# Kernel optimization log

Measured on AMD Instinct MI355X. Metric: run time of the kernel, lower is better.

Reference implementation:

```python
import jax, jax.numpy as jnp
import numpy as np

B_, L, DM = 2, 2048, 1024
DI, N, K, R = 2048, 16, 4, 64  # d_inner, d_state, d_conv, dt_rank


def setup_inputs() -> dict:
    key = jax.random.key(0)
    ks = jax.random.split(key, 8)
    return {
        "x": jax.random.normal(ks[0], (B_, L, DM), jnp.float32),
        "W_in": jax.random.normal(ks[1], (DM, 2 * DI), jnp.float32) * 0.02,
        "w_conv": jax.random.normal(ks[2], (DI, K), jnp.float32) * 0.1,
        "b_conv": jnp.zeros((DI,), jnp.float32),
        "W_x": jax.random.normal(ks[3], (DI, R + 2 * N), jnp.float32) * 0.02,
        "W_dt": jax.random.normal(ks[4], (R, DI), jnp.float32) * 0.02,
        "b_dt": jnp.full((DI,), -4.6, jnp.float32),  # softplus(b_dt) ~ 0.01 dt init
        "A_log": jnp.log(jnp.broadcast_to(jnp.arange(1, N + 1, dtype=jnp.float32), (DI, N))),
        "D": jnp.ones((DI,), jnp.float32),
        "W_out": jax.random.normal(ks[5], (DI, DM), jnp.float32) * 0.02,
        "gamma": jnp.ones((DM,), jnp.float32),
        "beta": jnp.zeros((DM,), jnp.float32),
    }


def reference(x, W_in, w_conv, b_conv, W_x, W_dt, b_dt, A_log, D, W_out, gamma, beta):
    Bb, Ll, Dm = x.shape
    Di, Kk = w_conv.shape
    Nn = A_log.shape[1]
    Rr = W_dt.shape[0]
    # in_proj -> (u, z)
    xz = x @ W_in  # [B,L,2*Di]
    u, z = jnp.split(xz, 2, axis=-1)
    # depthwise causal conv1d (kernel K, left pad K-1) + SiLU
    up = jnp.pad(u, ((0, 0), (Kk - 1, 0), (0, 0)))
    conv = b_conv + sum(up[:, k:k + Ll, :] * w_conv[:, k] for k in range(Kk))
    u = jax.nn.silu(conv)  # [B,L,Di]
    # x_proj -> dt, B, C
    dbc = u @ W_x
    dt, Bm, Cm = dbc[..., :Rr], dbc[..., Rr:Rr + Nn], dbc[..., Rr + Nn:]
    delta = jax.nn.softplus(dt @ W_dt + b_dt)  # [B,L,Di]
    A = -jnp.exp(A_log)  # [Di,N]

    def step(h, inputs):
        d_t, B_t, C_t, u_t = inputs  # [B,Di],[B,N],[B,N],[B,Di]
        dA = jnp.exp(d_t[..., None] * A)            # [B,Di,N]
        h = h * dA + (d_t * u_t)[..., None] * B_t[:, None, :]
        y = jnp.einsum('bdn,bn->bd', h, C_t)
        return h, y

    h0 = jnp.zeros((Bb, Di, Nn), x.dtype)
    _, ys = jax.lax.scan(step, h0, (delta.transpose(1, 0, 2), Bm.transpose(1, 0, 2),
                                    Cm.transpose(1, 0, 2), u.transpose(1, 0, 2)))
    y = ys.transpose(1, 0, 2)        # [B,L,Di]
    y = y + u * D                    # skip term
    y = y * jax.nn.silu(z)           # gate
    out = y @ W_out                  # [B,L,Dm]
    # LayerNorm
    mu = out.mean(-1, keepdims=True)
    var = ((out - mu) ** 2).mean(-1, keepdims=True)
    out = (out - mu) * jax.lax.rsqrt(var + 1e-5) * gamma + beta
    # dropout p=0 -> identity; residual
    return out + x
```

## Files before the change

kernel.cpp:

```cpp
#include <hip/hip_runtime.h>
#include <math.h>

#define L_SEQ 2048
#define DMOD  1024
#define DIN   2048
#define NBATCH 2
#define NTOK  (NBATCH * L_SEQ)
#define NST   16
#define RRANK 64
#define LOG2E 1.44269504088896f

#define GCHUNK 128
#define CLEN   (L_SEQ / GCHUNK)
#define SCHUNK 8
#define NSTAGE (CLEN / SCHUNK)

#define G4_KS   4
#define G4_KC   (2048 / G4_KS)
#define G2_KS   16
#define G2_KC   (2048 / G2_KS)

typedef __attribute__((ext_vector_type(8))) short  short8;
typedef __attribute__((ext_vector_type(4))) float  f32x4;

__device__ __forceinline__ ushort f2bf(float f) {
    unsigned u = __float_as_uint(f);
    u += 0x7fffu + ((u >> 16) & 1u);
    return (ushort)(u >> 16);
}
__device__ __forceinline__ float bf2f(ushort u) {
    return __uint_as_float(((unsigned)u) << 16);
}
__device__ __forceinline__ float fexp2(float x) {
    return __builtin_amdgcn_exp2f(x);
}

__device__ __forceinline__ void gload16(const ushort* g, ushort* l) {
    __builtin_amdgcn_global_load_lds(
        (const __attribute__((address_space(1))) unsigned int*)g,
        (__attribute__((address_space(3))) unsigned int*)l,
        16, 0, 0);
}

__device__ __forceinline__ void cast_body(
    const float* __restrict__ src, ushort* __restrict__ dst, int bid, int tid)
{
    int i = (bid * 256 + tid) * 8;
    float4 a = *(const float4*)(src + i);
    float4 b = *(const float4*)(src + i + 4);
    ushort4 o0 = make_ushort4(f2bf(a.x), f2bf(a.y), f2bf(a.z), f2bf(a.w));
    ushort4 o1 = make_ushort4(f2bf(b.x), f2bf(b.y), f2bf(b.z), f2bf(b.w));
    *(ushort4*)(dst + i)     = o0;
    *(ushort4*)(dst + i + 4) = o1;
}

__device__ __forceinline__ void tcast_body(
    const float* __restrict__ src, ushort* __restrict__ dst,
    int R, int C, int bx, int by, int tid)
{
    __shared__ float t[32][33];
    int tx = tid & 31;
    int ty = tid >> 5;
    int c0 = bx * 32;
    int r0 = by * 32;
    #pragma unroll
    for (int i = 0; i < 4; ++i)
        t[ty + i * 8][tx] = src[(size_t)(r0 + ty + i * 8) * C + c0 + tx];
    __syncthreads();
    #pragma unroll
    for (int i = 0; i < 4; ++i)
        dst[(size_t)(c0 + ty + i * 8) * R + r0 + tx] = f2bf(t[tx][ty + i * 8]);
}

__global__ __launch_bounds__(256) void prep_k(
    const float* __restrict__ x, const float* __restrict__ W_in,
    const float* __restrict__ W_dt, const float* __restrict__ W_x,
    const float* __restrict__ W_out,
    ushort* __restrict__ xb, ushort* __restrict__ Wib,
    ushort* __restrict__ Wdtb, ushort* __restrict__ Wxb,
    ushort* __restrict__ Wob)
{
    int bid = blockIdx.x, tid = threadIdx.x;
    if (bid < 2048) {
        cast_body(x, xb, bid, tid);
    } else if (bid < 6144) {
        int t = bid - 2048;
        tcast_body(W_in, Wib, 1024, 4096, t & 127, t >> 7, tid);
    } else if (bid < 6272) {
        int t = bid - 6144;
        tcast_body(W_dt, Wdtb, 64, 2048, t & 63, t >> 6, tid);
    } else if (bid < 6464) {
        int t = bid - 6272;
        tcast_body(W_x, Wxb, 2048, 96, t % 3, t / 3, tid);
    } else {
        int t = bid - 6464;
        tcast_body(W_out, Wob, 2048, 1024, t & 31, t >> 5, tid);
    }
}

__global__ __launch_bounds__(512, 2) void gemm8p(
    const ushort* __restrict__ A,
    const ushort* __restrict__ Bt,
    ushort* __restrict__ C,
    int K, int kslice, int ldc, size_t zstride,
    ushort* __restrict__ C2, int nsplit)
{
    __shared__ ushort lds[65536];

    const int tid  = threadIdx.x;
    const int wave = tid >> 6;
    const int lane = tid & 63;
    const int wr   = wave >> 2;
    const int wc   = wave & 3;

    const int gx = gridDim.x;
    int flat = blockIdx.y * gx + blockIdx.x;
    const int cpx = (gx * gridDim.y) >> 3;
    flat = (flat & 7) * cpx + (flat >> 3);
    const int bx = flat % gx;
    const int by = flat / gx;
    const int m0 = by * 256;
    const int n0 = bx * 256;
    const int kbeg = blockIdx.z * kslice;
    const int NH   = kslice >> 5;

    const int rr  = tid >> 2;
    const int gsw = ((tid & 3) ^ ((tid >> 3) & 3)) * 8;
    const ushort* a0 = A  + (size_t)(m0 + rr)        * K + kbeg + gsw;
    const ushort* a1 = A  + (size_t)(m0 + 128 + rr)  * K + kbeg + gsw;
    const ushort* b0 = Bt + (size_t)(n0 + rr)        * K + kbeg + gsw;
    const ushort* b1 = Bt + (size_t)(n0 + 128 + rr)  * K + kbeg + gsw;

    #define STAGE_H(op_, h_) do {                                              \
        const int ko_ = (h_) * 32;                                             \
        ushort* l_ = lds + ((h_) & 3) * 16384 + (op_) * 8192 + wave * 512;     \
        if ((op_) == 0) { gload16(a0 + ko_, l_); gload16(a1 + ko_, l_ + 4096); }\
        else            { gload16(b0 + ko_, l_); gload16(b1 + ko_, l_ + 4096); }\
    } while (0)

    const int lr  = lane & 15;
    const int swr = ((lane >> 4) ^ ((lr >> 1) & 3)) * 8;

    #define LDAH(i_, h_) (*(const short8*)&lds[((h_) & 3) * 16384              \
        + (wr * 128 + (i_) * 16 + lr) * 32 + swr])
    #define LDBH(j_, h_) (*(const short8*)&lds[((h_) & 3) * 16384 + 8192       \
        + (wc * 64 + (j_) * 16 + lr) * 32 + swr])

    f32x4 acc[8][4];
    #pragma unroll
    for (int i = 0; i < 8; ++i)
        #pragma unroll
        for (int j = 0; j < 4; ++j)
            acc[i][j] = (f32x4){0.f, 0.f, 0.f, 0.f};

    STAGE_H(0, 0); STAGE_H(1, 0);
    STAGE_H(0, 1); STAGE_H(1, 1);
    STAGE_H(0, 2); STAGE_H(1, 2);
    asm volatile("s_waitcnt vmcnt(8)" ::: "memory");
    __builtin_amdgcn_s_barrier();

    short8 a_[4], b_[4];

    for (int h = 0; h < NH; ++h) {
        const bool st = (h + 3 < NH);

        #pragma unroll
        for (int i = 0; i < 4; ++i) a_[i] = LDAH(i, h);
        #pragma unroll
        for (int j = 0; j < 4; ++j) b_[j] = LDBH(j, h);
        if (st) STAGE_H(0, h + 3);
        __builtin_amdgcn_s_barrier();
        asm volatile("s_waitcnt lgkmcnt(0)" ::: "memory");
        __builtin_amdgcn_sched_barrier(0);
        __builtin_amdgcn_s_setprio(1);
        #pragma unroll
        for (int i = 0; i < 4; ++i)
            #pragma unroll
            for (int j = 0; j < 4; ++j)
                acc[i][j] = __builtin_amdgcn_mfma_f32_16x16x32_bf16(
                    a_[i], b_[j], acc[i][j], 0, 0, 0);
        __builtin_amdgcn_s_setprio(0);
        __builtin_amdgcn_s_barrier();

        #pragma unroll
        for (int i = 0; i < 4; ++i) a_[i] = LDAH(4 + i, h);
        if (st) STAGE_H(1, h + 3);
        if (h + 4 <= NH - 1)
            asm volatile("s_waitcnt vmcnt(8)" ::: "memory");
        else if (h + 3 == NH - 1)
            asm volatile("s_waitcnt vmcnt(4)" ::: "memory");
        else
            asm volatile("s_waitcnt vmcnt(0)" ::: "memory");
        __builtin_amdgcn_s_barrier();
        asm volatile("s_waitcnt lgkmcnt(0)" ::: "memory");
        __builtin_amdgcn_sched_barrier(0);
        __builtin_amdgcn_s_setprio(1);
        #pragma unroll
        for (int i = 0; i < 4; ++i)
            #pragma unroll
            for (int j = 0; j < 4; ++j)
                acc[4 + i][j] = __builtin_amdgcn_mfma_f32_16x16x32_bf16(
                    a_[i], b_[j], acc[4 + i][j], 0, 0, 0);
        __builtin_amdgcn_s_setprio(0);
        __builtin_amdgcn_s_barrier();
    }
    #undef STAGE_H
    #undef LDAH
    #undef LDBH

    ushort* Cp = C + (size_t)blockIdx.z * zstride;
    int ncol = n0;
    if (C2 != nullptr && n0 >= nsplit) { Cp = C2; ncol = n0 - nsplit; }
    const int rb = m0 + wr * 128 + ((lane >> 4) << 2);
    const int cb = ncol + wc * 64 + lr;
    #pragma unroll
    for (int i = 0; i < 8; ++i)
        #pragma unroll
        for (int j = 0; j < 4; ++j)
            #pragma unroll
            for (int r = 0; r < 4; ++r)
                Cp[(size_t)(rb + i * 16 + r) * ldc + cb + j * 16] =
                    f2bf(acc[i][j][r]);
}

template<int EPI, int OBF>
__global__ __launch_bounds__(256) void gemm_mfma(
    const ushort* __restrict__ A,
    const ushort* __restrict__ Bt,
    void* __restrict__ Cv,
    int M, int N, int K, int ldc, const float* __restrict__ bias)
{
    __shared__ ushort As[128 * 32];
    __shared__ ushort Bs[128 * 32];

    const int tid  = threadIdx.x;
    const int wave = tid >> 6;
    const int lane = tid & 63;
    const int wm   = (wave & 1) * 64;
    const int wn   = (wave >> 1) * 64;
    const int m0   = blockIdx.y * 128;
    const int n0   = blockIdx.x * 128;

    const int srow = lane >> 2;
    const int sg   = (lane & 3) ^ ((srow >> 1) & 3);
    const ushort* gA0 = A  + (size_t)(m0 + wave * 32 + srow)      * K + sg * 8;
    const ushort* gA1 = A  + (size_t)(m0 + wave * 32 + 16 + srow) * K + sg * 8;
    const ushort* gB0 = Bt + (size_t)(n0 + wave * 32 + srow)      * K + sg * 8;
    const ushort* gB1 = Bt + (size_t)(n0 + wave * 32 + 16 + srow) * K + sg * 8;
    ushort* lA0 = As + (wave * 32)      * 32;
    ushort* lA1 = As + (wave * 32 + 16) * 32;
    ushort* lB0 = Bs + (wave * 32)      * 32;
    ushort* lB1 = Bs + (wave * 32 + 16) * 32;

    const int lrow = lane & 15;
    const int swr  = ((lane >> 4) ^ ((lrow >> 1) & 3)) * 8;

    f32x4 acc[4][4];
    #pragma unroll
    for (int i = 0; i < 4; ++i)
        #pragma unroll
        for (int j = 0; j < 4; ++j)
            acc[i][j] = (f32x4){0.f, 0.f, 0.f, 0.f};

    for (int k0 = 0; k0 < K; k0 += 32) {
        __syncthreads();
        gload16(gA0 + k0, lA0);
        gload16(gA1 + k0, lA1);
        gload16(gB0 + k0, lB0);
        gload16(gB1 + k0, lB1);
        __syncthreads();

        short8 af[4], bfr[4];
        #pragma unroll
        for (int i = 0; i < 4; ++i) {
            af[i]  = *(const short8*)&As[(wm + i * 16 + lrow) * 32 + swr];
            bfr[i] = *(const short8*)&Bs[(wn + i * 16 + lrow) * 32 + swr];
        }
        #pragma unroll
        for (int i = 0; i < 4; ++i)
            #pragma unroll
            for (int j = 0; j < 4; ++j)
                acc[i][j] = __builtin_amdgcn_mfma_f32_16x16x32_bf16(
                    af[i], bfr[j], acc[i][j], 0, 0, 0);
    }

    const int rb = m0 + wm + ((lane >> 4) << 2);
    const int cb = n0 + wn + lrow;

    float bias4[4];
    if (EPI == 1) {
        #pragma unroll
        for (int j = 0; j < 4; ++j) bias4[j] = bias[cb + j * 16];
    }

    #pragma unroll
    for (int i = 0; i < 4; ++i)
        #pragma unroll
        for (int j = 0; j < 4; ++j)
            #pragma unroll
            for (int r = 0; r < 4; ++r) {
                float v = acc[i][j][r];
                int col = cb + j * 16;
                if (EPI == 1) {
                    v += bias4[j];
                    if (v <= 20.f) {
                        float t = fexp2(v * LOG2E);
                        v = __builtin_amdgcn_logf(1.f + t) * (1.f / LOG2E);
                    }
                }
                size_t off = (size_t)(rb + i * 16 + r) * ldc + col;
                if (OBF) ((ushort*)Cv)[off] = f2bf(v);
                else     ((float*)Cv)[off]  = v;
            }
}

__global__ __launch_bounds__(256) void gemm2_mfma(
    const ushort* __restrict__ A,
    const ushort* __restrict__ Bt,
    float* __restrict__ part)
{
    __shared__ ushort As[128 * 32];
    __shared__ ushort Bs[128 * 32];

    const int K = 2048;
    const int tid  = threadIdx.x;
    const int wave = tid >> 6;
    const int lane = tid & 63;
    const int wm   = (wave & 1) * 64;
    const int wn   = (wave >> 1) * 64;
    const int m0   = blockIdx.x * 128;
    const int ks   = blockIdx.z;

    const int srow = lane >> 2;
    const int sg   = (lane & 3) ^ ((srow >> 1) & 3);
    int rB0 = wave * 32 + srow;      if (rB0 > 95) rB0 = 95;
    int rB1 = wave * 32 + 16 + srow; if (rB1 > 95) rB1 = 95;
    const ushort* gA0 = A  + (size_t)(m0 + wave * 32 + srow)      * K + sg * 8;
    const ushort* gA1 = A  + (size_t)(m0 + wave * 32 + 16 + srow) * K + sg * 8;
    const ushort* gB0 = Bt + (size_t)rB0 * K + sg * 8;
    const ushort* gB1 = Bt + (size_t)rB1 * K + sg * 8;
    ushort* lA0 = As + (wave * 32)      * 32;
    ushort* lA1 = As + (wave * 32 + 16) * 32;
    ushort* lB0 = Bs + (wave * 32)      * 32;
    ushort* lB1 = Bs + (wave * 32 + 16) * 32;

    const int lrow = lane & 15;
    const int swr  = ((lane >> 4) ^ ((lrow >> 1) & 3)) * 8;

    f32x4 acc[4][4];
    #pragma unroll
    for (int i = 0; i < 4; ++i)
        #pragma unroll
        for (int j = 0; j < 4; ++j)
            acc[i][j] = (f32x4){0.f, 0.f, 0.f, 0.f};

    const int kbeg = ks * G2_KC, kend = kbeg + G2_KC;
    for (int k0 = kbeg; k0 < kend; k0 += 32) {
        __syncthreads();
        gload16(gA0 + k0, lA0);
        gload16(gA1 + k0, lA1);
        gload16(gB0 + k0, lB0);
        gload16(gB1 + k0, lB1);
        __syncthreads();

        short8 af[4], bfr[4];
        #pragma unroll
        for (int i = 0; i < 4; ++i) {
            af[i]  = *(const short8*)&As[(wm + i * 16 + lrow) * 32 + swr];
            bfr[i] = *(const short8*)&Bs[(wn + i * 16 + lrow) * 32 + swr];
        }
        #pragma unroll
        for (int i = 0; i < 4; ++i)
            #pragma unroll
            for (int j = 0; j < 4; ++j)
                acc[i][j] = __builtin_amdgcn_mfma_f32_16x16x32_bf16(
                    af[i], bfr[j], acc[i][j], 0, 0, 0);
    }

    float* po = part + (size_t)ks * NTOK * 96;
    const int rb = m0 + wm + ((lane >> 4) << 2);
    const int cb = wn + lrow;
    #pragma unroll
    for (int i = 0; i < 4; ++i)
        #pragma unroll
        for (int j = 0; j < 4; ++j) {
            int col = cb + j * 16;
            if (col < 96) {
                #pragma unroll
                for (int r = 0; r < 4; ++r)
                    po[(size_t)(rb + i * 16 + r) * 96 + col] = acc[i][j][r];
            }
        }
}

__global__ __launch_bounds__(256) void gemm2_reduce_dt(
    const float* __restrict__ part, float* __restrict__ dbc,
    ushort* __restrict__ dtb)
{
    int i = (blockIdx.x * 256 + threadIdx.x) * 4;
    float4 s = *(const float4*)(part + i);
    #pragma unroll
    for (int ks = 1; ks < G2_KS; ++ks) {
        float4 v = *(const float4*)(part + (size_t)ks * NTOK * 96 + i);
        s.x += v.x; s.y += v.y; s.z += v.z; s.w += v.w;
    }
    *(float4*)(dbc + i) = s;
    int col = i % 96;
    if (col < RRANK) {
        int row = i / 96;
        ushort* q = dtb + (size_t)row * RRANK + col;
        q[0] = f2bf(s.x); q[1] = f2bf(s.y); q[2] = f2bf(s.z); q[3] = f2bf(s.w);
    }
}

__global__ __launch_bounds__(256) void conv_silu_k(
    const ushort* __restrict__ up, const float* __restrict__ w_conv,
    const float* __restrict__ b_conv, ushort* __restrict__ ub)
{
    const int token = blockIdx.x;
    const int d     = threadIdx.x * 8;
    const int t     = token & (L_SEQ - 1);

    float4 w[8];
    const float4* pw = (const float4*)(w_conv + (size_t)d * 4);
    #pragma unroll
    for (int i = 0; i < 8; ++i) w[i] = pw[i];

    float acc[8];
    {
        float4 bc0 = *(const float4*)(b_conv + d);
        float4 bc1 = *(const float4*)(b_conv + d + 4);
        acc[0] = bc0.x; acc[1] = bc0.y; acc[2] = bc0.z; acc[3] = bc0.w;
        acc[4] = bc1.x; acc[5] = bc1.y; acc[6] = bc1.z; acc[7] = bc1.w;
    }

    #pragma unroll
    for (int k = 0; k < 4; ++k) {
        int tt = t - 3 + k;
        if (tt >= 0) {
            short8 v = *(const short8*)(up + (size_t)(token - 3 + k) * 2048 + d);
            #pragma unroll
            for (int i = 0; i < 8; ++i)
                acc[i] += bf2f((ushort)v[i]) * (&w[i].x)[k];
        }
    }

    short8 o;
    #pragma unroll
    for (int i = 0; i < 8; ++i) {
        float s = acc[i] / (1.f + __expf(-acc[i]));
        o[i] = (short)f2bf(s);
    }
    *(short8*)(ub + (size_t)token * DIN + d) = o;
}

__global__ __launch_bounds__(256) void scan_part1(
    const float* __restrict__ dlt,
    const ushort* __restrict__ ub,
    const float* __restrict__ dbc,
    const float* __restrict__ A_log,
    float* __restrict__ c_out,
    float* __restrict__ dsum_out)
{
    int chunk = blockIdx.x & (GCHUNK - 1);
    int dg    = (blockIdx.x >> 7) & 7;
    int b     = blockIdx.x >> 10;
    int wave  = threadIdx.x >> 6;
    int lane  = threadIdx.x & 63;
    int d     = dg * 256 + wave * 64 + lane;

    __shared__ float sB[4][SCHUNK][16];

    float Al[NST];
    const float4* pA = (const float4*)(A_log + (size_t)d * NST);
    #pragma unroll
    for (int q = 0; q < 4; ++q) {
        float4 a = pA[q];
        Al[q*4+0] = -__expf(a.x) * LOG2E;
        Al[q*4+1] = -__expf(a.y) * LOG2E;
        Al[q*4+2] = -__expf(a.z) * LOG2E;
        Al[q*4+3] = -__expf(a.w) * LOG2E;
    }

    float h[NST];
    #pragma unroll
    for (int n = 0; n < NST; ++n) h[n] = 0.f;
    float dsum = 0.f;

    const size_t tokbase = (size_t)b * L_SEQ + (size_t)chunk * CLEN;
    const float*  pD = dlt + tokbase * 2048 + d;
    const ushort* pU = ub  + tokbase * 2048 + d;
    const float*  pB = dbc + tokbase * 96 + RRANK;

    float rd[2][SCHUNK], ru[2][SCHUNK], rb[2][2];

    #pragma unroll
    for (int i = 0; i < SCHUNK; ++i) {
        rd[0][i] = pD[(size_t)i * 2048];
        ru[0][i] = bf2f(pU[(size_t)i * 2048]);
    }
    #pragma unroll
    for (int i = 0; i < 2; ++i) {
        int e = i * 64 + lane;
        rb[0][i] = pB[(size_t)(e >> 4) * 96 + (e & 15)];
    }

    #pragma unroll
    for (int st = 0; st < NSTAGE; ++st) {
        const int cur = st & 1, nxt = cur ^ 1;
        #pragma unroll
        for (int i = 0; i < 2; ++i) {
            int e = i * 64 + lane;
            sB[wave][e >> 4][e & 15] = rb[cur][i];
        }
        if (st + 1 < NSTAGE) {
            const size_t to = (size_t)(st + 1) * SCHUNK;
            #pragma unroll
            for (int i = 0; i < SCHUNK; ++i) {
                rd[nxt][i] = pD[(to + i) * 2048];
                ru[nxt][i] = bf2f(pU[(to + i) * 2048]);
            }
            #pragma unroll
            for (int i = 0; i < 2; ++i) {
                int e = i * 64 + lane;
                rb[nxt][i] = pB[(to + (e >> 4)) * 96 + (e & 15)];
            }
        }
        #pragma unroll
        for (int s = 0; s < SCHUNK; ++s) {
            float delta = rd[cur][s];
            float du    = delta * ru[cur][s];
            dsum += delta;
            #pragma unroll
            for (int q = 0; q < 4; ++q) {
                float4 bq = *(const float4*)&sB[wave][s][q * 4];
                h[q*4+0] = h[q*4+0] * fexp2(delta * Al[q*4+0]) + du * bq.x;
                h[q*4+1] = h[q*4+1] * fexp2(delta * Al[q*4+1]) + du * bq.y;
                h[q*4+2] = h[q*4+2] * fexp2(delta * Al[q*4+2]) + du * bq.z;
                h[q*4+3] = h[q*4+3] * fexp2(delta * Al[q*4+3]) + du * bq.w;
            }
        }
    }

    size_t base = (((size_t)b * DIN + d) * GCHUNK + chunk) * NST;
    #pragma unroll
    for (int q = 0; q < 4; ++q)
        *(float4*)&c_out[base + q * 4] = make_float4(h[q*4], h[q*4+1], h[q*4+2], h[q*4+3]);
    dsum_out[((size_t)b * DIN + d) * GCHUNK + chunk] = dsum;
}

__global__ __launch_bounds__(256) void scan_part2(
    float* __restrict__ cbuf,
    const float* __restrict__ dsum_in,
    const float* __restrict__ A_log)
{
    int idx = blockIdx.x * 256 + threadIdx.x;
    int n   = idx & 15;
    int d   = (idx >> 4) & (DIN - 1);
    int b   = idx >> 15;

    float Al = -__expf(A_log[(size_t)d * NST + n]) * LOG2E;
    size_t cb = ((size_t)b * DIN + d) * GCHUNK;

    float h = 0.f;
    for (int ch = 0; ch < GCHUNK; ++ch) {
        size_t o = (cb + ch) * NST + n;
        float c  = cbuf[o];
        float dA = fexp2(Al * dsum_in[cb + ch]);
        cbuf[o]  = h;
        h = h * dA + c;
    }
}

__global__ __launch_bounds__(256) void scan_part3(
    const float* __restrict__ dlt,
    const ushort* __restrict__ zb,
    ushort* __restrict__ ub,
    const float* __restrict__ dbc,
    const float* __restrict__ A_log,
    const float* __restrict__ Dp,
    const float* __restrict__ h_start)
{
    int chunk = blockIdx.x & (GCHUNK - 1);
    int dg    = (blockIdx.x >> 7) & 7;
    int b     = blockIdx.x >> 10;
    int wave  = threadIdx.x >> 6;
    int lane  = threadIdx.x & 63;
    int d     = dg * 256 + wave * 64 + lane;

    __shared__ float sBC[4][SCHUNK][32];

    float Al[NST];
    const float4* pA = (const float4*)(A_log + (size_t)d * NST);
    #pragma unroll
    for (int q = 0; q < 4; ++q) {
        float4 a = pA[q];
        Al[q*4+0] = -__expf(a.x) * LOG2E;
        Al[q*4+1] = -__expf(a.y) * LOG2E;
        Al[q*4+2] = -__expf(a.z) * LOG2E;
        Al[q*4+3] = -__expf(a.w) * LOG2E;
    }
    float Dd = Dp[d];

    float h[NST];
    size_t hb = (((size_t)b * DIN + d) * GCHUNK + chunk) * NST;
    #pragma unroll
    for (int q = 0; q < 4; ++q) {
        float4 v = *(const float4*)&h_start[hb + q * 4];
        h[q*4] = v.x; h[q*4+1] = v.y; h[q*4+2] = v.z; h[q*4+3] = v.w;
    }

    const size_t tokbase = (size_t)b * L_SEQ + (size_t)chunk * CLEN;
    const float*  pD = dlt + tokbase * 2048 + d;
    const ushort* pZ = zb  + tokbase * 2048 + d;
    ushort*       pU = ub  + tokbase * 2048 + d;
    const float*  pB = dbc + tokbase * 96 + RRANK;

    float rd[2][SCHUNK], ru[2][SCHUNK], rz[2][SCHUNK], rb[2][4];

    #pragma unroll
    for (int i = 0; i < SCHUNK; ++i) {
        rd[0][i] = pD[(size_t)i * 2048];
        ru[0][i] = bf2f(pU[(size_t)i * 2048]);
        rz[0][i] = bf2f(pZ[(size_t)i * 2048]);
    }
    #pragma unroll
    for (int i = 0; i < 4; ++i) {
        int e = i * 64 + lane;
        rb[0][i] = pB[(size_t)(e >> 5) * 96 + (e & 31)];
    }

    #pragma unroll
    for (int st = 0; st < NSTAGE; ++st) {
        const int cur = st & 1, nxt = cur ^ 1;
        #pragma unroll
        for (int i = 0; i < 4; ++i) {
            int e = i * 64 + lane;
            sBC[wave][e >> 5][e & 31] = rb[cur][i];
        }
        if (st + 1 < NSTAGE) {
            const size_t to = (size_t)(st + 1) * SCHUNK;
            #pragma unroll
            for (int i = 0; i < SCHUNK; ++i) {
                rd[nxt][i] = pD[(to + i) * 2048];
                ru[nxt][i] = bf2f(pU[(to + i) * 2048]);
                rz[nxt][i] = bf2f(pZ[(to + i) * 2048]);
            }
            #pragma unroll
            for (int i = 0; i < 4; ++i) {
                int e = i * 64 + lane;
                rb[nxt][i] = pB[(to + (e >> 5)) * 96 + (e & 31)];
            }
        }
        #pragma unroll
        for (int s = 0; s < SCHUNK; ++s) {
            float delta = rd[cur][s];
            float u     = ru[cur][s];
            float du    = delta * u;
            float y = 0.f;
            #pragma unroll
            for (int q = 0; q < 4; ++q) {
                float4 bq = *(const float4*)&sBC[wave][s][q * 4];
                float4 cq = *(const float4*)&sBC[wave][s][16 + q * 4];
                h[q*4+0] = h[q*4+0] * fexp2(delta * Al[q*4+0]) + du * bq.x; y += h[q*4+0] * cq.x;
                h[q*4+1] = h[q*4+1] * fexp2(delta * Al[q*4+1]) + du * bq.y; y += h[q*4+1] * cq.y;
                h[q*4+2] = h[q*4+2] * fexp2(delta * Al[q*4+2]) + du * bq.z; y += h[q*4+2] * cq.z;
                h[q*4+3] = h[q*4+3] * fexp2(delta * Al[q*4+3]) + du * bq.w; y += h[q*4+3] * cq.w;
            }
            float z  = rz[cur][s];
            float sz = z / (1.f + __expf(-z));
            pU[((size_t)st * SCHUNK + s) * 2048] = f2bf((y + u * Dd) * sz);
        }
    }
}

__global__ __launch_bounds__(256) void ln4_k(
    const ushort* __restrict__ part,
    const float* __restrict__ x,
    const float* __restrict__ gamma, const float* __restrict__ beta,
    float* __restrict__ out)
{
    int row = blockIdx.x;
    int tid = threadIdx.x;
    const size_t off = (size_t)row * DMOD + tid * 4;

    float4 v = {0.f, 0.f, 0.f, 0.f};
    #pragma unroll
    for (int ks = 0; ks < G4_KS; ++ks) {
        ushort4 p = *(const ushort4*)(part + (size_t)ks * NTOK * DMOD + off);
        v.x += bf2f(p.x); v.y += bf2f(p.y); v.z += bf2f(p.z); v.w += bf2f(p.w);
    }

    float s  = v.x + v.y + v.z + v.w;
    float s2 = v.x * v.x + v.y * v.y + v.z * v.z + v.w * v.w;
    #pragma unroll
    for (int off2 = 32; off2 > 0; off2 >>= 1) {
        s  += __shfl_down(s, off2);
        s2 += __shfl_down(s2, off2);
    }
    __shared__ float ws[4], ws2[4];
    int wave = tid >> 6, lane = tid & 63;
    if (lane == 0) { ws[wave] = s; ws2[wave] = s2; }
    __syncthreads();
    if (tid == 0) {
        float ts = 0.f, ts2 = 0.f;
        #pragma unroll
        for (int w = 0; w < 4; ++w) { ts += ws[w]; ts2 += ws2[w]; }
        ws[0] = ts; ws2[0] = ts2;
    }
    __syncthreads();
    float mu  = ws[0] * (1.f / DMOD);
    float var = ws2[0] * (1.f / DMOD) - mu * mu;
    float rs  = rsqrtf(var + 1e-5f);

    float4 g  = ((const float4*)gamma)[tid];
    float4 be = ((const float4*)beta)[tid];
    float4 xr = *(const float4*)(x + off);
    float4 o;
    o.x = (v.x - mu) * rs * g.x + be.x + xr.x;
    o.y = (v.y - mu) * rs * g.y + be.y + xr.y;
    o.z = (v.z - mu) * rs * g.z + be.z + xr.z;
    o.w = (v.w - mu) * rs * g.w + be.w + xr.w;
    *(float4*)(out + off) = o;
}

extern "C" void kernel_launch(void* const* d_in, const int* in_sizes, int n_in,
                              void* d_out, int out_size, void* d_ws, size_t ws_size,
                              hipStream_t stream)
{
    const float* x      = (const float*)d_in[0];
    const float* W_in   = (const float*)d_in[1];
    const float* w_conv = (const float*)d_in[2];
    const float* b_conv = (const float*)d_in[3];
    const float* W_x    = (const float*)d_in[4];
    const float* W_dt   = (const float*)d_in[5];
    const float* b_dt   = (const float*)d_in[6];
    const float* A_log  = (const float*)d_in[7];
    const float* Dp     = (const float*)d_in[8];
    const float* W_out  = (const float*)d_in[9];
    const float* gamma  = (const float*)d_in[10];
    const float* beta   = (const float*)d_in[11];
    float* out = (float*)d_out;

    char* ws = (char*)d_ws;
    const size_t MB = 1024 * 1024;
    ushort* zb     = (ushort*)(ws);
    ushort* ub     = (ushort*)(ws + 16 * MB);
    float*  dlt    = (float*)(ws + 32 * MB);
    float*  dbc    = (float*)(ws + 64 * MB);
    ushort* Wdtb   = (ushort*)(ws + 65 * MB + 512 * 1024);
    ushort* Wxb    = (ushort*)(ws + 65 * MB + 768 * 1024);
    ushort* dtb    = (ushort*)(ws + 66 * MB + 128 * 1024);
    float*  dsum   = (float*)(ws + 67 * MB);
    ushort* Wob    = (ushort*)(ws + 69 * MB);
    float*  c_buf  = (float*)(ws + 73 * MB);
    ushort* xb     = (ushort*)(ws + 73 * MB);
    ushort* Wib    = (ushort*)(ws + 81 * MB);
    ushort* ub_pre = (ushort*)(ws + 89 * MB);
    float*  g2part = (float*)(ws + 73 * MB);
    ushort* g4part = (ushort*)(ws + 32 * MB);

    dim3 blk(256);

    prep_k<<<dim3(8512), blk, 0, stream>>>(x, W_in, W_dt, W_x, W_out,
                                           xb, Wib, Wdtb, Wxb, Wob);
    gemm8p<<<dim3(16, 16, 1), dim3(512), 0, stream>>>(
        xb, Wib, ub_pre, 1024, 1024, 2048, 0, zb, 2048);
    conv_silu_k<<<dim3(NTOK), blk, 0, stream>>>(ub_pre, w_conv, b_conv, ub);
    gemm2_mfma<<<dim3(32, 1, G2_KS), blk, 0, stream>>>(ub, Wxb, g2part);
    gemm2_reduce_dt<<<dim3(NTOK * 96 / 4 / 256), blk, 0, stream>>>(g2part, dbc, dtb);
    gemm_mfma<1, 0><<<dim3(16, 32), blk, 0, stream>>>(
        dtb, Wdtb, dlt, 4096, 2048, 64, 2048, b_dt);
    scan_part1<<<dim3(NBATCH * 8 * GCHUNK), blk, 0, stream>>>(
        dlt, ub, dbc, A_log, c_buf, dsum);
    scan_part2<<<dim3(NBATCH * DIN * NST / 256), blk, 0, stream>>>(
        c_buf, dsum, A_log);
    scan_part3<<<dim3(NBATCH * 8 * GCHUNK), blk, 0, stream>>>(
        dlt, zb, ub, dbc, A_log, Dp, c_buf);
    gemm8p<<<dim3(4, 16, G4_KS), dim3(512), 0, stream>>>(
        ub, Wob, g4part, 2048, G4_KC, DMOD, (size_t)NTOK * DMOD,
        nullptr, 0x7fffffff);
    ln4_k<<<dim3(NTOK), blk, 0, stream>>>(g4part, x, gamma, beta, out);
}
```

Baseline: 319.2 us.

## Software-pipeline LDS fragment loads with MFMA using double-buffered registers

Restructures the 256x256 bf16 GEMM main loop into pairs of k-steps with ping-pong register fragments (aLo/aHi, bE/bO). The next half-tile's LDS reads are issued before the current MFMA block runs, and partial lgkmcnt waits replace full drains, so LDS latency overlaps with matrix math. This raises register pressure and assumes NH is even. The waitcnt bookkeeping is more fragile.

```diff
diff --git a/kernel.cpp b/kernel.cpp
--- a/kernel.cpp
+++ b/kernel.cpp
@@ -128,14 +128,14 @@
     const int gsw = ((tid & 3) ^ ((tid >> 3) & 3)) * 8;
     const ushort* a0 = A  + (size_t)(m0 + rr)        * K + kbeg + gsw;
     const ushort* a1 = A  + (size_t)(m0 + 128 + rr)  * K + kbeg + gsw;
-    const ushort* b0 = Bt + (size_t)(n0 + rr)        * K + kbeg + gsw;
-    const ushort* b1 = Bt + (size_t)(n0 + 128 + rr)  * K + kbeg + gsw;
+    const ushort* b0p = Bt + (size_t)(n0 + rr)       * K + kbeg + gsw;
+    const ushort* b1p = Bt + (size_t)(n0 + 128 + rr) * K + kbeg + gsw;
 
     #define STAGE_H(op_, h_) do {                                              \
         const int ko_ = (h_) * 32;                                             \
         ushort* l_ = lds + ((h_) & 3) * 16384 + (op_) * 8192 + wave * 512;     \
-        if ((op_) == 0) { gload16(a0 + ko_, l_); gload16(a1 + ko_, l_ + 4096); }\
-        else            { gload16(b0 + ko_, l_); gload16(b1 + ko_, l_ + 4096); }\
+        if ((op_) == 0) { gload16(a0 + ko_, l_);  gload16(a1 + ko_, l_ + 4096); }\
+        else            { gload16(b0p + ko_, l_); gload16(b1p + ko_, l_ + 4096); }\
     } while (0)
 
     const int lr  = lane & 15;
@@ -145,6 +145,26 @@
         + (wr * 128 + (i_) * 16 + lr) * 32 + swr])
     #define LDBH(j_, h_) (*(const short8*)&lds[((h_) & 3) * 16384 + 8192       \
         + (wc * 64 + (j_) * 16 + lr) * 32 + swr])
+
+    #define MFMA16(as_, bs_, off_) do {                                        \
+        __builtin_amdgcn_s_setprio(1);                                         \
+        _Pragma("unroll")                                                      \
+        for (int i = 0; i < 4; ++i)                                            \
+            _Pragma("unroll")                                                  \
+            for (int j = 0; j < 4; ++j)                                        \
+                acc[(off_) + i][j] = __builtin_amdgcn_mfma_f32_16x16x32_bf16(  \
+                    as_[i], bs_[j], acc[(off_) + i][j], 0, 0, 0);              \
+        __builtin_amdgcn_s_setprio(0);                                         \
+    } while (0)
+
+    #define VMC_B(h_) do {                                                     \
+        if ((h_) + 3 < NH)                                                     \
+            asm volatile("s_waitcnt vmcnt(8)" ::: "memory");                   \
+        else if ((h_) + 2 < NH)                                                \
+            asm volatile("s_waitcnt vmcnt(4)" ::: "memory");                   \
+        else                                                                   \
+            asm volatile("s_waitcnt vmcnt(0)" ::: "memory");                   \
+    } while (0)
 
     f32x4 acc[8][4];
     #pragma unroll
@@ -159,54 +179,66 @@
     asm volatile("s_waitcnt vmcnt(8)" ::: "memory");
     __builtin_amdgcn_s_barrier();
 
-    short8 a_[4], b_[4];
-
-    for (int h = 0; h < NH; ++h) {
-        const bool st = (h + 3 < NH);
-
-        #pragma unroll
-        for (int i = 0; i < 4; ++i) a_[i] = LDAH(i, h);
-        #pragma unroll
-        for (int j = 0; j < 4; ++j) b_[j] = LDBH(j, h);
-        if (st) STAGE_H(0, h + 3);
+    short8 aLo[4], aHi[4], bE[4], bO[4];
+    #pragma unroll
+    for (int i = 0; i < 4; ++i) aLo[i] = LDAH(i, 0);
+    #pragma unroll
+    for (int j = 0; j < 4; ++j) bE[j]  = LDBH(j, 0);
+
+    for (int hp = 0; hp < NH / 2; ++hp) {
+        const int h0 = 2 * hp, h1 = 2 * hp + 1;
+
+        if (h0 + 3 < NH) STAGE_H(0, h0 + 3);
         __builtin_amdgcn_s_barrier();
-        asm volatile("s_waitcnt lgkmcnt(0)" ::: "memory");
+        #pragma unroll
+        for (int i = 0; i < 4; ++i) aHi[i] = LDAH(4 + i, h0);
+        asm volatile("s_waitcnt lgkmcnt(4)" ::: "memory");
         __builtin_amdgcn_sched_barrier(0);
-        __builtin_amdgcn_s_setprio(1);
-        #pragma unroll
-        for (int i = 0; i < 4; ++i)
-            #pragma unroll
-            for (int j = 0; j < 4; ++j)
-                acc[i][j] = __builtin_amdgcn_mfma_f32_16x16x32_bf16(
-                    a_[i], b_[j], acc[i][j], 0, 0, 0);
-        __builtin_amdgcn_s_setprio(0);
+        MFMA16(aLo, bE, 0);
         __builtin_amdgcn_s_barrier();
 
-        #pragma unroll
-        for (int i = 0; i < 4; ++i) a_[i] = LDAH(4 + i, h);
-        if (st) STAGE_H(1, h + 3);
-        if (h + 4 <= NH - 1)
-            asm volatile("s_waitcnt vmcnt(8)" ::: "memory");
-        else if (h + 3 == NH - 1)
-            asm volatile("s_waitcnt vmcnt(4)" ::: "memory");
-        else
-            asm volatile("s_waitcnt vmcnt(0)" ::: "memory");
+        if (h0 + 3 < NH) STAGE_H(1, h0 + 3);
+        VMC_B(h0);
         __builtin_amdgcn_s_barrier();
-        asm volatile("s_waitcnt lgkmcnt(0)" ::: "memory");
+        #pragma unroll
+        for (int i = 0; i < 4; ++i) aLo[i] = LDAH(i, h1);
+        #pragma unroll
+        for (int j = 0; j < 4; ++j) bO[j]  = LDBH(j, h1);
+        asm volatile("s_waitcnt lgkmcnt(8)" ::: "memory");
         __builtin_amdgcn_sched_barrier(0);
-        __builtin_amdgcn_s_setprio(1);
-        #pragma unroll
-        for (int i = 0; i < 4; ++i)
-            #pragma unroll
-            for (int j = 0; j < 4; ++j)
-                acc[4 + i][j] = __builtin_amdgcn_mfma_f32_16x16x32_bf16(
-                    a_[i], b_[j], acc[4 + i][j], 0, 0, 0);
-        __builtin_amdgcn_s_setprio(0);
+        MFMA16(aHi, bE, 4);
+        __builtin_amdgcn_s_barrier();
+
+        if (h1 + 3 < NH) STAGE_H(0, h1 + 3);
+        __builtin_amdgcn_s_barrier();
+        #pragma unroll
+        for (int i = 0; i < 4; ++i) aHi[i] = LDAH(4 + i, h1);
+        asm volatile("s_waitcnt lgkmcnt(4)" ::: "memory");
+        __builtin_amdgcn_sched_barrier(0);
+        MFMA16(aLo, bO, 0);
+        __builtin_amdgcn_s_barrier();
+
+        if (h1 + 3 < NH) STAGE_H(1, h1 + 3);
+        VMC_B(h1);
+        __builtin_amdgcn_s_barrier();
+        if (h1 + 1 < NH) {
+            #pragma unroll
+            for (int i = 0; i < 4; ++i) aLo[i] = LDAH(i, h1 + 1);
+            #pragma unroll
+            for (int j = 0; j < 4; ++j) bE[j]  = LDBH(j, h1 + 1);
+            asm volatile("s_waitcnt lgkmcnt(8)" ::: "memory");
+        } else {
+            asm volatile("s_waitcnt lgkmcnt(0)" ::: "memory");
+        }
+        __builtin_amdgcn_sched_barrier(0);
+        MFMA16(aHi, bO, 4);
         __builtin_amdgcn_s_barrier();
     }
     #undef STAGE_H
     #undef LDAH
     #undef LDBH
+    #undef MFMA16
+    #undef VMC_B
 
     ushort* Cp = C + (size_t)blockIdx.z * zstride;
     int ncol = n0;
```

New measurement: 316.5 us. No clear change (-0.8%).
